# Optimization experiments

Hardware: AMD Instinct MI355X
Metric: run time of the kernel (lower is better)

Reference implementation:

```python
import jax, jax.numpy as jnp
import numpy as np

N = 1024
H = 128
W = 128
TANX = 0.5
TANY = 0.5
FX = W / (2.0 * TANX)
FY = H / (2.0 * TANY)
SCALE_MOD = 1.0

# spherical-harmonic constants (match 3DGS CUDA)
C0 = 0.28209479177387814
C1 = 0.4886025119029199
C2 = (1.0925484305920792, -1.0925484305920792, 0.31539156525252005, -1.0925484305920792, 0.5462742152960396)
C3 = (-0.5900435899266435, 2.890611442640554, -0.4570457994644658, 0.3731763325901154, -0.4570457994644658, 1.445305721320277, -0.5900435899266435)


def _quat_to_rot(q):
    q = q / jnp.linalg.norm(q, axis=-1, keepdims=True)
    r, x, y, z = q[:, 0], q[:, 1], q[:, 2], q[:, 3]
    row0 = jnp.stack([1 - 2 * (y * y + z * z), 2 * (x * y - r * z), 2 * (x * z + r * y)], -1)
    row1 = jnp.stack([2 * (x * y + r * z), 1 - 2 * (x * x + z * z), 2 * (y * z - r * x)], -1)
    row2 = jnp.stack([2 * (x * z - r * y), 2 * (y * z + r * x), 1 - 2 * (x * x + y * y)], -1)
    return jnp.stack([row0, row1, row2], 1)  # [n,3,3]


def _sh_to_rgb(sh, d):
    x, y, z = d[:, 0:1], d[:, 1:2], d[:, 2:3]
    res = C0 * sh[:, 0]
    res = res - C1 * y * sh[:, 1] + C1 * z * sh[:, 2] - C1 * x * sh[:, 3]
    xx, yy, zz = x * x, y * y, z * z
    xy, yz, xz = x * y, y * z, x * z
    res = (res + C2[0] * xy * sh[:, 4] + C2[1] * yz * sh[:, 5]
           + C2[2] * (2 * zz - xx - yy) * sh[:, 6] + C2[3] * xz * sh[:, 7]
           + C2[4] * (xx - yy) * sh[:, 8])
    res = (res + C3[0] * y * (3 * xx - yy) * sh[:, 9] + C3[1] * xy * z * sh[:, 10]
           + C3[2] * y * (4 * zz - xx - yy) * sh[:, 11]
           + C3[3] * z * (2 * zz - 3 * xx - 3 * yy) * sh[:, 12]
           + C3[4] * x * (4 * zz - xx - yy) * sh[:, 13]
           + C3[5] * z * (xx - yy) * sh[:, 14] + C3[6] * x * (xx - 3 * yy) * sh[:, 15])
    return jnp.maximum(res + 0.5, 0.0)


def _rasterize(means3D, opacities, shs, scales, rotations, viewmatrix, projmatrix, campos, bg):
    n = means3D.shape[0]
    dt = means3D.dtype
    hom = jnp.concatenate([means3D, jnp.ones((n, 1), dt)], -1)
    p_view = hom @ viewmatrix                      # row-vector convention
    depth = p_view[:, 2]
    valid = depth > 0.2
    p_hom = hom @ projmatrix
    p_proj = p_hom[:, :3] / (p_hom[:, 3:4] + 1e-7)
    # 3D covariance: Sigma = R diag(s^2) R^T
    R = _quat_to_rot(rotations)
    M = R * (scales * SCALE_MOD)[:, None, :]
    Sigma = jnp.einsum('nij,nkj->nik', M, M)
    # EWA projection to 2D covariance
    tz = jnp.where(valid, depth, 1.0)
    txtz = jnp.clip(p_view[:, 0] / tz, -1.3 * TANX, 1.3 * TANX) * tz
    tytz = jnp.clip(p_view[:, 1] / tz, -1.3 * TANY, 1.3 * TANY) * tz
    zero = jnp.zeros_like(tz)
    J = jnp.stack([
        jnp.stack([FX / tz, zero, -FX * txtz / (tz * tz)], -1),
        jnp.stack([zero, FY / tz, -FY * tytz / (tz * tz)], -1)], 1)  # [n,2,3]
    Wr = viewmatrix[:3, :3].T
    T2 = jnp.einsum('nij,jk->nik', J, Wr)
    cov2 = jnp.einsum('nij,njk,nlk->nil', T2, Sigma, T2)
    a = cov2[:, 0, 0] + 0.3
    b = cov2[:, 0, 1]
    c = cov2[:, 1, 1] + 0.3
    det = a * c - b * b
    valid = valid & (det > 0)
    inv_det = 1.0 / jnp.where(det > 0, det, 1.0)
    conA, conB, conC = c * inv_det, -b * inv_det, a * inv_det
    mid = 0.5 * (a + c)
    lam1 = mid + jnp.sqrt(jnp.maximum(0.1, mid * mid - det))
    radii = jnp.where(valid, jnp.ceil(3.0 * jnp.sqrt(lam1)), 0.0).astype(jnp.int32)
    # NDC -> pixel centers (ndc2Pix)
    xy = ((p_proj[:, :2] + 1.0) * jnp.array([W, H], dt) - 1.0) * 0.5
    # SH evaluation -> RGB
    dirs = means3D - campos[None, :]
    dirs = dirs / jnp.linalg.norm(dirs, axis=-1, keepdims=True)
    colors = _sh_to_rgb(shs, dirs)                 # [n,3]
    # global front-to-back depth sort
    order = jnp.argsort(jnp.where(valid, depth, jnp.inf))
    conA, conB, conC = conA[order], conB[order], conC[order]
    xyo = xy[order]
    opo = opacities[order, 0]
    colo = colors[order]
    vo = valid[order]
    # dense per-pixel evaluation (tile binning is a perf optimization only)
    yy, xx = jnp.meshgrid(jnp.arange(H, dtype=dt), jnp.arange(W, dtype=dt), indexing='ij')
    pxf = xx.reshape(-1)
    pyf = yy.reshape(-1)
    dx = xyo[:, 0:1] - pxf[None, :]                # [n, HW]
    dy = xyo[:, 1:2] - pyf[None, :]
    power = -0.5 * (conA[:, None] * dx * dx + conC[:, None] * dy * dy) - conB[:, None] * dx * dy
    alpha = jnp.minimum(0.99, opo[:, None] * jnp.exp(jnp.minimum(power, 0.0)))
    alpha = jnp.where((power <= 0) & (alpha >= 1.0 / 255.0) & vo[:, None], alpha, 0.0)
    Tinc = jnp.cumprod(1.0 - alpha, axis=0)        # T after gaussian i
    Texc = jnp.concatenate([jnp.ones((1, H * W), dt), Tinc[:-1]], 0)  # T before gaussian i
    ae = jnp.where(Tinc >= 1e-4, alpha, 0.0)       # early-termination threshold as in CUDA
    weight = Texc * ae
    img = jnp.einsum('np,nc->cp', weight, colo)
    Tfin = jnp.prod(1.0 - ae, axis=0)
    img = img + bg[:, None] * Tfin[None, :]
    return img.reshape(3, H, W), radii


def setup_inputs() -> dict:
    key = jax.random.key(0)
    ks = jax.random.split(key, 6)
    means3D = jax.random.uniform(ks[0], (N, 3)) * jnp.array([4.0, 4.0, 4.0]) + jnp.array([-2.0, -2.0, 2.0])
    means2D = jnp.zeros((N, 3), jnp.float32)
    opacities = jax.random.uniform(ks[1], (N, 1)) * 0.8 + 0.2
    shs = jax.random.normal(ks[2], (N, 16, 3)) * 0.3
    scales = jax.random.uniform(ks[3], (N, 3)) * 0.1 + 0.02
    rotations = jax.random.normal(ks[4], (N, 4))
    viewmatrix = jnp.eye(4, dtype=jnp.float32)     # camera at origin looking +z
    znear, zfar = 0.01, 100.0
    projmatrix = jnp.array([[1.0 / TANX, 0, 0, 0],
                            [0, 1.0 / TANY, 0, 0],
                            [0, 0, zfar / (zfar - znear), 1.0],
                            [0, 0, -zfar * znear / (zfar - znear), 0]], jnp.float32)
    campos = jnp.zeros(3, jnp.float32)
    bg = jnp.zeros(3, jnp.float32)
    return {"means3D": means3D, "means2D": means2D, "opacities": opacities, "shs": shs,
            "scales": scales, "rotations": rotations, "viewmatrix": viewmatrix,
            "projmatrix": projmatrix, "campos": campos, "bg": bg}


def reference(means3D, means2D, opacities, shs, scales, rotations, viewmatrix, projmatrix, campos, bg):
    color, radii = _rasterize(means3D, opacities, shs, scales, rotations, viewmatrix, projmatrix, campos, bg)
    return color, radii
```

## Files before the change

### kernel.cpp

```cpp
#include <hip/hip_runtime.h>
#include <stdint.h>

#define N_G   1024
#define H_IMG 128
#define W_IMG 128
#define TILE  8
#define TILES_X (W_IMG / TILE)
#define N_TILES (TILES_X * (H_IMG/TILE))
#define NT    256
#define FXc   128.0f
#define FYc   128.0f

__global__ __launch_bounds__(NT) void gauss_tile_kernel(
    const float* __restrict__ means3D, const float* __restrict__ opac,
    const float* __restrict__ shs,     const float* __restrict__ scales,
    const float* __restrict__ rot,     const float* __restrict__ vm,
    const float* __restrict__ pm,      const float* __restrict__ campos,
    const float* __restrict__ bg,
    float* __restrict__ out)
{
    __shared__ float gxA[N_G], gyA[N_G], cAA[N_G], cBA[N_G], cCA[N_G],
                     opA[N_G], rcA[N_G];
    __shared__ unsigned int dpA[N_G];
    __shared__ unsigned long long keys[N_G];
    __shared__ float colR[N_G], colG[N_G], colB[N_G];
    __shared__ int cnt;

    const int t   = threadIdx.x;
    const int bid = blockIdx.x;
    const int tx = bid & (TILES_X - 1), ty = bid / TILES_X;
    const float x0 = (float)(tx * TILE), x1 = x0 + (float)(TILE - 1);
    const float y0 = (float)(ty * TILE), y1 = y0 + (float)(TILE - 1);

    if (t == 0) cnt = 0;

    for (int k = 0; k < N_G / NT; ++k) {
        const int n = k * NT + t;

        float mx = means3D[n*3+0], my = means3D[n*3+1], mz = means3D[n*3+2];

        float pv0   = mx*vm[0] + my*vm[4] + mz*vm[8]  + vm[12];
        float pv1   = mx*vm[1] + my*vm[5] + mz*vm[9]  + vm[13];
        float depth = mx*vm[2] + my*vm[6] + mz*vm[10] + vm[14];
        bool dvalid = depth > 0.2f;

        float ph0 = mx*pm[0] + my*pm[4] + mz*pm[8]  + pm[12];
        float ph1 = mx*pm[1] + my*pm[5] + mz*pm[9]  + pm[13];
        float ph3 = mx*pm[3] + my*pm[7] + mz*pm[11] + pm[15];
        float invw = 1.0f / (ph3 + 1e-7f);
        float pp0 = ph0 * invw, pp1 = ph1 * invw;

        float4 q = *(const float4*)(rot + n*4);
        float qn = sqrtf(q.x*q.x + q.y*q.y + q.z*q.z + q.w*q.w);
        float qr = q.x/qn, qx = q.y/qn, qy = q.z/qn, qz = q.w/qn;
        float R00 = 1.f - 2.f*(qy*qy + qz*qz), R01 = 2.f*(qx*qy - qr*qz), R02 = 2.f*(qx*qz + qr*qy);
        float R10 = 2.f*(qx*qy + qr*qz), R11 = 1.f - 2.f*(qx*qx + qz*qz), R12 = 2.f*(qy*qz - qr*qx);
        float R20 = 2.f*(qx*qz - qr*qy), R21 = 2.f*(qy*qz + qr*qx), R22 = 1.f - 2.f*(qx*qx + qy*qy);

        float s0 = scales[n*3+0], s1 = scales[n*3+1], s2 = scales[n*3+2];
        float M00=R00*s0, M01=R01*s1, M02=R02*s2;
        float M10=R10*s0, M11=R11*s1, M12=R12*s2;
        float M20=R20*s0, M21=R21*s1, M22=R22*s2;

        float S00 = M00*M00 + M01*M01 + M02*M02;
        float S01 = M00*M10 + M01*M11 + M02*M12;
        float S02 = M00*M20 + M01*M21 + M02*M22;
        float S11 = M10*M10 + M11*M11 + M12*M12;
        float S12 = M10*M20 + M11*M21 + M12*M22;
        float S22 = M20*M20 + M21*M21 + M22*M22;

        float tz   = dvalid ? depth : 1.0f;
        float txtz = fminf(fmaxf(pv0 / tz, -0.65f), 0.65f) * tz;
        float tytz = fminf(fmaxf(pv1 / tz, -0.65f), 0.65f) * tz;
        float J00 = FXc / tz, J02 = -FXc * txtz / (tz*tz);
        float J11 = FYc / tz, J12 = -FYc * tytz / (tz*tz);

        float T20k0 = J00*vm[0] + J02*vm[2];
        float T20k1 = J00*vm[4] + J02*vm[6];
        float T20k2 = J00*vm[8] + J02*vm[10];
        float T21k0 = J11*vm[1] + J12*vm[2];
        float T21k1 = J11*vm[5] + J12*vm[6];
        float T21k2 = J11*vm[9] + J12*vm[10];

        float U00 = T20k0*S00 + T20k1*S01 + T20k2*S02;
        float U01 = T20k0*S01 + T20k1*S11 + T20k2*S12;
        float U02 = T20k0*S02 + T20k1*S12 + T20k2*S22;
        float U10 = T21k0*S00 + T21k1*S01 + T21k2*S02;
        float U11 = T21k0*S01 + T21k1*S11 + T21k2*S12;
        float U12 = T21k0*S02 + T21k1*S12 + T21k2*S22;
        float cov00 = U00*T20k0 + U01*T20k1 + U02*T20k2;
        float cov01 = U00*T21k0 + U01*T21k1 + U02*T21k2;
        float cov11 = U10*T21k0 + U11*T21k1 + U12*T21k2;

        float a = cov00 + 0.3f, b = cov01, c = cov11 + 0.3f;
        float det = a*c - b*b;
        bool valid = dvalid && (det > 0.0f);
        float inv_det = (det > 0.0f) ? (1.0f / det) : 1.0f;

        float mid  = 0.5f * (a + c);
        float lam1 = mid + sqrtf(fmaxf(0.1f, mid*mid - det));
        if (bid == 0)
            out[3*H_IMG*W_IMG + n] = valid ? ceilf(3.0f * sqrtf(lam1)) : 0.0f;

        float op = opac[n];
        float op255 = op * 255.0f;
        float rc2 = (valid && op255 > 1.0f) ? (2.0f * logf(op255) * lam1 * 1.01f + 1.0f)
                                            : -1.0f;

        gxA[n] = ((pp0 + 1.0f) * (float)W_IMG - 1.0f) * 0.5f;
        gyA[n] = ((pp1 + 1.0f) * (float)H_IMG - 1.0f) * 0.5f;
        cAA[n] = c * inv_det;
        cBA[n] = -b * inv_det;
        cCA[n] = a * inv_det;
        opA[n] = op;
        rcA[n] = rc2;
        dpA[n] = __float_as_uint(depth);
    }
    __syncthreads();

    for (int k = 0; k < N_G / NT; ++k) {
        const int n = k * NT + t;
        float gx = gxA[n], gy = gyA[n];
        float cx = fminf(fmaxf(gx, x0), x1) - gx;
        float cy = fminf(fmaxf(gy, y0), y1) - gy;
        if (cx*cx + cy*cy <= rcA[n]) {
            int slot = atomicAdd(&cnt, 1);
            keys[slot] = ((unsigned long long)dpA[n] << 32) | (unsigned int)n;
        }
    }
    __syncthreads();
    const int M = cnt;

    int P = 1; while (P < M) P <<= 1;
    for (int i = M + t; i < P; i += NT) keys[i] = ~0ull;
    __syncthreads();
    for (int k = 2; k <= P; k <<= 1) {
        for (int j = k >> 1; j > 0; j >>= 1) {
            for (int i = t; i < P; i += NT) {
                int l = i ^ j;
                if (l > i) {
                    unsigned long long ka = keys[i], kb = keys[l];
                    bool asc = ((i & k) == 0);
                    if ((ka > kb) == asc) { keys[i] = kb; keys[l] = ka; }
                }
            }
            __syncthreads();
        }
    }

    const float cpx = campos[0], cpy = campos[1], cpz = campos[2];
    for (int s = t; s < M; s += NT) {
        int idx = (int)(keys[s] & 0xFFFFFFFFu);
        float mx = means3D[idx*3+0], my = means3D[idx*3+1], mz = means3D[idx*3+2];
        float dxm = mx - cpx, dym = my - cpy, dzm = mz - cpz;
        float dn = sqrtf(dxm*dxm + dym*dym + dzm*dzm);
        float sx = dxm/dn, sy = dym/dn, sz = dzm/dn;
        float xx = sx*sx, yy = sy*sy, zz = sz*sz;
        float xy = sx*sy, yz = sy*sz, xz = sx*sz;

        float bb[16];
        bb[0]  = 0.28209479177387814f;
        bb[1]  = -0.4886025119029199f * sy;
        bb[2]  =  0.4886025119029199f * sz;
        bb[3]  = -0.4886025119029199f * sx;
        bb[4]  =  1.0925484305920792f * xy;
        bb[5]  = -1.0925484305920792f * yz;
        bb[6]  =  0.31539156525252005f * (2.f*zz - xx - yy);
        bb[7]  = -1.0925484305920792f * xz;
        bb[8]  =  0.5462742152960396f * (xx - yy);
        bb[9]  = -0.5900435899266435f * sy * (3.f*xx - yy);
        bb[10] =  2.890611442640554f  * xy * sz;
        bb[11] = -0.4570457994644658f * sy * (4.f*zz - xx - yy);
        bb[12] =  0.3731763325901154f * sz * (2.f*zz - 3.f*xx - 3.f*yy);
        bb[13] = -0.4570457994644658f * sx * (4.f*zz - xx - yy);
        bb[14] =  1.445305721320277f  * sz * (xx - yy);
        bb[15] = -0.5900435899266435f * sx * (xx - 3.f*yy);

        float acc[3] = {0.f, 0.f, 0.f};
        const float4* sh4 = (const float4*)(shs + idx*48);
        #pragma unroll
        for (int u = 0; u < 12; ++u) {
            float4 v = sh4[u];
            int f = 4*u;
            acc[(f+0)%3] += bb[(f+0)/3] * v.x;
            acc[(f+1)%3] += bb[(f+1)/3] * v.y;
            acc[(f+2)%3] += bb[(f+2)/3] * v.z;
            acc[(f+3)%3] += bb[(f+3)/3] * v.w;
        }
        colR[s] = fmaxf(acc[0] + 0.5f, 0.f);
        colG[s] = fmaxf(acc[1] + 0.5f, 0.f);
        colB[s] = fmaxf(acc[2] + 0.5f, 0.f);
    }
    __syncthreads();

    if (t < 64) {
        const float px = x0 + (float)(t & (TILE - 1));
        const float py = y0 + (float)(t / TILE);
        float T = 1.0f, Tfin = 1.0f, cr = 0.f, cg = 0.f, cb = 0.f;
        bool live = true;

        for (int j = 0; j < M; ++j) {
            int idx = (int)(keys[j] & 0xFFFFFFFFu);
            float gx = gxA[idx], gy = gyA[idx];
            float A  = cAA[idx], B  = cBA[idx], C = cCA[idx], op = opA[idx];
            float dx = gx - px, dy = gy - py;
            float power = -0.5f * (A*dx*dx + C*dy*dy) - B*dx*dy;
            float alpha = fminf(0.99f, op * __expf(power));
            if (live && power <= 0.0f && alpha >= (1.0f/255.0f)) {
                float Tnew = T * (1.0f - alpha);
                if (Tnew < 1e-4f) {
                    live = false;
                } else {
                    float w = T * alpha;
                    cr += w * colR[j]; cg += w * colG[j]; cb += w * colB[j];
                    Tfin *= (1.0f - alpha);
                    T = Tnew;
                }
            }
            if (__ballot(live) == 0ull) break;
        }

        int p = (int)py * W_IMG + (int)px;
        out[p]                 = cr + bg[0] * Tfin;
        out[H_IMG*W_IMG + p]   = cg + bg[1] * Tfin;
        out[2*H_IMG*W_IMG + p] = cb + bg[2] * Tfin;
    }
}

extern "C" void kernel_launch(void* const* d_in, const int* in_sizes, int n_in,
                              void* d_out, int out_size, void* d_ws, size_t ws_size,
                              hipStream_t stream) {
    const float* means3D = (const float*)d_in[0];
    const float* opac    = (const float*)d_in[2];
    const float* shs     = (const float*)d_in[3];
    const float* scales  = (const float*)d_in[4];
    const float* rot     = (const float*)d_in[5];
    const float* vm      = (const float*)d_in[6];
    const float* pm      = (const float*)d_in[7];
    const float* campos  = (const float*)d_in[8];
    const float* bg      = (const float*)d_in[9];

    gauss_tile_kernel<<<N_TILES, NT, 0, stream>>>(
        means3D, opac, shs, scales, rot, vm, pm, campos, bg, (float*)d_out);
}
```

Baseline: 89.72 us.

## Replace bitonic sort with rank sort and chunked packed-record blending with early exit

Fuses tile culling into the preprocessing loop, replaces the multi-barrier bitonic sort with an O(M^2) rank-counting sort, and processes sorted gaussians in chunks of 256. For each chunk it evaluates SH colors only for that chunk and packs all per-gaussian blending parameters into contiguous shared records, so blending reads vectorized records instead of doing indirect gathers. When all pixels saturate, the block stops early and skips color evaluation for later chunks. The rank sort is quadratic in the per-tile count and could cost more when tiles hold many gaussians.

```diff
diff --git a/kernel.cpp b/kernel.cpp
--- a/kernel.cpp
+++ b/kernel.cpp
@@ -8,6 +8,7 @@
 #define TILES_X (W_IMG / TILE)
 #define N_TILES (TILES_X * (H_IMG/TILE))
 #define NT    256
+#define CHUNK 256
 #define FXc   128.0f
 #define FYc   128.0f
 
@@ -19,12 +20,11 @@
     const float* __restrict__ bg,
     float* __restrict__ out)
 {
-    __shared__ float gxA[N_G], gyA[N_G], cAA[N_G], cBA[N_G], cCA[N_G],
-                     opA[N_G], rcA[N_G];
-    __shared__ unsigned int dpA[N_G];
-    __shared__ unsigned long long keys[N_G];
-    __shared__ float colR[N_G], colG[N_G], colB[N_G];
-    __shared__ int cnt;
+    __shared__ float gxA[N_G], gyA[N_G], cAA[N_G], cBA[N_G], cCA[N_G], opA[N_G];
+    __shared__ unsigned long long svKeys[N_G];
+    __shared__ int   ranks[N_G];
+    __shared__ float srec[CHUNK * 12];
+    __shared__ int   cnt, allDead;
 
     const int t   = threadIdx.x;
     const int bid = blockIdx.x;
@@ -32,8 +32,10 @@
     const float x0 = (float)(tx * TILE), x1 = x0 + (float)(TILE - 1);
     const float y0 = (float)(ty * TILE), y1 = y0 + (float)(TILE - 1);
 
-    if (t == 0) cnt = 0;
-
+    if (t == 0) { cnt = 0; allDead = 0; }
+    __syncthreads();
+
+    #pragma unroll
     for (int k = 0; k < N_G / NT; ++k) {
         const int n = k * NT + t;
 
@@ -102,124 +104,125 @@
         if (bid == 0)
             out[3*H_IMG*W_IMG + n] = valid ? ceilf(3.0f * sqrtf(lam1)) : 0.0f;
 
+        float gx = ((pp0 + 1.0f) * (float)W_IMG - 1.0f) * 0.5f;
+        float gy = ((pp1 + 1.0f) * (float)H_IMG - 1.0f) * 0.5f;
         float op = opac[n];
+
+        gxA[n] = gx; gyA[n] = gy;
+        cAA[n] = c * inv_det; cBA[n] = -b * inv_det; cCA[n] = a * inv_det;
+        opA[n] = op;
+
         float op255 = op * 255.0f;
         float rc2 = (valid && op255 > 1.0f) ? (2.0f * logf(op255) * lam1 * 1.01f + 1.0f)
                                             : -1.0f;
 
-        gxA[n] = ((pp0 + 1.0f) * (float)W_IMG - 1.0f) * 0.5f;
-        gyA[n] = ((pp1 + 1.0f) * (float)H_IMG - 1.0f) * 0.5f;
-        cAA[n] = c * inv_det;
-        cBA[n] = -b * inv_det;
-        cCA[n] = a * inv_det;
-        opA[n] = op;
-        rcA[n] = rc2;
-        dpA[n] = __float_as_uint(depth);
-    }
-    __syncthreads();
-
-    for (int k = 0; k < N_G / NT; ++k) {
-        const int n = k * NT + t;
-        float gx = gxA[n], gy = gyA[n];
         float cx = fminf(fmaxf(gx, x0), x1) - gx;
         float cy = fminf(fmaxf(gy, y0), y1) - gy;
-        if (cx*cx + cy*cy <= rcA[n]) {
+        if (cx*cx + cy*cy <= rc2) {
             int slot = atomicAdd(&cnt, 1);
-            keys[slot] = ((unsigned long long)dpA[n] << 32) | (unsigned int)n;
+            svKeys[slot] = ((unsigned long long)__float_as_uint(depth) << 32) | (unsigned int)n;
         }
     }
     __syncthreads();
     const int M = cnt;
 
-    int P = 1; while (P < M) P <<= 1;
-    for (int i = M + t; i < P; i += NT) keys[i] = ~0ull;
+    for (int s = t; s < M; s += NT) {
+        unsigned long long key = svKeys[s];
+        int r = 0;
+        for (int j = 0; j < M; ++j)
+            r += (svKeys[j] < key) ? 1 : 0;
+        ranks[s] = r;
+    }
     __syncthreads();
-    for (int k = 2; k <= P; k <<= 1) {
-        for (int j = k >> 1; j > 0; j >>= 1) {
-            for (int i = t; i < P; i += NT) {
-                int l = i ^ j;
-                if (l > i) {
-                    unsigned long long ka = keys[i], kb = keys[l];
-                    bool asc = ((i & k) == 0);
-                    if ((ka > kb) == asc) { keys[i] = kb; keys[l] = ka; }
+
+    const float cpx = campos[0], cpy = campos[1], cpz = campos[2];
+    const float px = x0 + (float)(t & (TILE - 1));
+    const float py = y0 + (float)((t >> 3) & (TILE - 1));
+    float T = 1.0f, Tfin = 1.0f, cr = 0.f, cg = 0.f, cb = 0.f;
+    bool live = true;
+
+    for (int base = 0; base < M; base += CHUNK) {
+        for (int s = t; s < M; s += NT) {
+            int r = ranks[s] - base;
+            if (r >= 0 && r < CHUNK) {
+                int idx = (int)(svKeys[s] & 0xFFFFFFFFu);
+
+                float mx = means3D[idx*3+0], my = means3D[idx*3+1], mz = means3D[idx*3+2];
+                float dxm = mx - cpx, dym = my - cpy, dzm = mz - cpz;
+                float dn = sqrtf(dxm*dxm + dym*dym + dzm*dzm);
+                float sx = dxm/dn, sy = dym/dn, sz = dzm/dn;
+                float xx = sx*sx, yy = sy*sy, zz = sz*sz;
+                float xy = sx*sy, yz = sy*sz, xz = sx*sz;
+                float bb[16];
+                bb[0]  = 0.28209479177387814f;
+                bb[1]  = -0.4886025119029199f * sy;
+                bb[2]  =  0.4886025119029199f * sz;
+                bb[3]  = -0.4886025119029199f * sx;
+                bb[4]  =  1.0925484305920792f * xy;
+                bb[5]  = -1.0925484305920792f * yz;
+                bb[6]  =  0.31539156525252005f * (2.f*zz - xx - yy);
+                bb[7]  = -1.0925484305920792f * xz;
+                bb[8]  =  0.5462742152960396f * (xx - yy);
+                bb[9]  = -0.5900435899266435f * sy * (3.f*xx - yy);
+                bb[10] =  2.890611442640554f  * xy * sz;
+                bb[11] = -0.4570457994644658f * sy * (4.f*zz - xx - yy);
+                bb[12] =  0.3731763325901154f * sz * (2.f*zz - 3.f*xx - 3.f*yy);
+                bb[13] = -0.4570457994644658f * sx * (4.f*zz - xx - yy);
+                bb[14] =  1.445305721320277f  * sz * (xx - yy);
+                bb[15] = -0.5900435899266435f * sx * (xx - 3.f*yy);
+
+                float acc0 = 0.f, acc1 = 0.f, acc2 = 0.f;
+                const float4* sh4 = (const float4*)(shs + idx*48);
+                #pragma unroll
+                for (int u = 0; u < 12; ++u) {
+                    float4 v = sh4[u];
+                    const int f = 4*u;
+                    if ((f+0)%3==0) acc0 += bb[(f+0)/3]*v.x; else if ((f+0)%3==1) acc1 += bb[(f+0)/3]*v.x; else acc2 += bb[(f+0)/3]*v.x;
+                    if ((f+1)%3==0) acc0 += bb[(f+1)/3]*v.y; else if ((f+1)%3==1) acc1 += bb[(f+1)/3]*v.y; else acc2 += bb[(f+1)/3]*v.y;
+                    if ((f+2)%3==0) acc0 += bb[(f+2)/3]*v.z; else if ((f+2)%3==1) acc1 += bb[(f+2)/3]*v.z; else acc2 += bb[(f+2)/3]*v.z;
+                    if ((f+3)%3==0) acc0 += bb[(f+3)/3]*v.w; else if ((f+3)%3==1) acc1 += bb[(f+3)/3]*v.w; else acc2 += bb[(f+3)/3]*v.w;
                 }
+
+                float* rp = srec + r * 12;
+                rp[0] = gxA[idx]; rp[1] = gyA[idx]; rp[2] = cAA[idx]; rp[3] = cBA[idx];
+                rp[4] = cCA[idx]; rp[5] = opA[idx];
+                rp[6] = fmaxf(acc0 + 0.5f, 0.f);
+                rp[7] = fmaxf(acc1 + 0.5f, 0.f);
+                rp[8] = fmaxf(acc2 + 0.5f, 0.f);
             }
-            __syncthreads();
         }
-    }
-
-    const float cpx = campos[0], cpy = campos[1], cpz = campos[2];
-    for (int s = t; s < M; s += NT) {
-        int idx = (int)(keys[s] & 0xFFFFFFFFu);
-        float mx = means3D[idx*3+0], my = means3D[idx*3+1], mz = means3D[idx*3+2];
-        float dxm = mx - cpx, dym = my - cpy, dzm = mz - cpz;
-        float dn = sqrtf(dxm*dxm + dym*dym + dzm*dzm);
-        float sx = dxm/dn, sy = dym/dn, sz = dzm/dn;
-        float xx = sx*sx, yy = sy*sy, zz = sz*sz;
-        float xy = sx*sy, yz = sy*sz, xz = sx*sz;
-
-        float bb[16];
-        bb[0]  = 0.28209479177387814f;
-        bb[1]  = -0.4886025119029199f * sy;
-        bb[2]  =  0.4886025119029199f * sz;
-        bb[3]  = -0.4886025119029199f * sx;
-        bb[4]  =  1.0925484305920792f * xy;
-        bb[5]  = -1.0925484305920792f * yz;
-        bb[6]  =  0.31539156525252005f * (2.f*zz - xx - yy);
-        bb[7]  = -1.0925484305920792f * xz;
-        bb[8]  =  0.5462742152960396f * (xx - yy);
-        bb[9]  = -0.5900435899266435f * sy * (3.f*xx - yy);
-        bb[10] =  2.890611442640554f  * xy * sz;
-        bb[11] = -0.4570457994644658f * sy * (4.f*zz - xx - yy);
-        bb[12] =  0.3731763325901154f * sz * (2.f*zz - 3.f*xx - 3.f*yy);
-        bb[13] = -0.4570457994644658f * sx * (4.f*zz - xx - yy);
-        bb[14] =  1.445305721320277f  * sz * (xx - yy);
-        bb[15] = -0.5900435899266435f * sx * (xx - 3.f*yy);
-
-        float acc[3] = {0.f, 0.f, 0.f};
-        const float4* sh4 = (const float4*)(shs + idx*48);
-        #pragma unroll
-        for (int u = 0; u < 12; ++u) {
-            float4 v = sh4[u];
-            int f = 4*u;
-            acc[(f+0)%3] += bb[(f+0)/3] * v.x;
-            acc[(f+1)%3] += bb[(f+1)/3] * v.y;
-            acc[(f+2)%3] += bb[(f+2)/3] * v.z;
-            acc[(f+3)%3] += bb[(f+3)/3] * v.w;
+        __syncthreads();
+
+        if (t < 64) {
+            int nb = min(CHUNK, M - base);
+            for (int j = 0; j < nb; ++j) {
+                const float* g = srec + j * 12;
+                float4 g0 = *(const float4*)(g);
+                float4 g1 = *(const float4*)(g + 4);
+                float  b2 = g[8];
+                float dx = g0.x - px, dy = g0.y - py;
+                float power = -0.5f * (g0.z*dx*dx + g1.x*dy*dy) - g0.w*dx*dy;
+                float alpha = fminf(0.99f, g1.y * __expf(power));
+                if (live && power <= 0.0f && alpha >= (1.0f/255.0f)) {
+                    float Tnew = T * (1.0f - alpha);
+                    if (Tnew < 1e-4f) {
+                        live = false;
+                    } else {
+                        float w = T * alpha;
+                        cr += w * g1.z; cg += w * g1.w; cb += w * b2;
+                        Tfin *= (1.0f - alpha);
+                        T = Tnew;
+                    }
+                }
+                if (__ballot(live) == 0ull) break;
+            }
+            if (__ballot(live) == 0ull && t == 0) allDead = 1;
         }
-        colR[s] = fmaxf(acc[0] + 0.5f, 0.f);
-        colG[s] = fmaxf(acc[1] + 0.5f, 0.f);
-        colB[s] = fmaxf(acc[2] + 0.5f, 0.f);
-    }
-    __syncthreads();
+        __syncthreads();
+        if (allDead) break;
+    }
 
     if (t < 64) {
-        const float px = x0 + (float)(t & (TILE - 1));
-        const float py = y0 + (float)(t / TILE);
-        float T = 1.0f, Tfin = 1.0f, cr = 0.f, cg = 0.f, cb = 0.f;
-        bool live = true;
-
-        for (int j = 0; j < M; ++j) {
-            int idx = (int)(keys[j] & 0xFFFFFFFFu);
-            float gx = gxA[idx], gy = gyA[idx];
-            float A  = cAA[idx], B  = cBA[idx], C = cCA[idx], op = opA[idx];
-            float dx = gx - px, dy = gy - py;
-            float power = -0.5f * (A*dx*dx + C*dy*dy) - B*dx*dy;
-            float alpha = fminf(0.99f, op * __expf(power));
-            if (live && power <= 0.0f && alpha >= (1.0f/255.0f)) {
-                float Tnew = T * (1.0f - alpha);
-                if (Tnew < 1e-4f) {
-                    live = false;
-                } else {
-                    float w = T * alpha;
-                    cr += w * colR[j]; cg += w * colG[j]; cb += w * colB[j];
-                    Tfin *= (1.0f - alpha);
-                    T = Tnew;
-                }
-            }
-            if (__ballot(live) == 0ull) break;
-        }
-
         int p = (int)py * W_IMG + (int)px;
         out[p]                 = cr + bg[0] * Tfin;
         out[H_IMG*W_IMG + p]   = cg + bg[1] * Tfin;
```

Measured after the change: 88.36 us. Within noise of the previous version (-1.5%).
